# Kernel optimization log

Measured on AMD Instinct MI355X. Metric: run time of the kernel, lower is better.

The kernel has to match this reference:

```python
import jax, jax.numpy as jnp
import numpy as np

N = 100000
E = 3200000
F_IN = 16
H = 128
LAT = 64
L = 3
G = 1024


def setup_inputs() -> dict:
    key = jax.random.key(0)
    ks = jax.random.split(key, 12)
    x = jax.random.normal(ks[0], (N, F_IN), dtype=jnp.float32)
    edge_index = jax.random.randint(ks[1], (2, E), 0, N, dtype=jnp.int64)
    batch = jnp.sort(jax.random.randint(ks[2], (N,), 0, G, dtype=jnp.int64))
    batch = batch.at[-1].set(G - 1)  # ensure batch.max()+1 == G
    s_in = 1.0 / np.sqrt(F_IN)
    s_h = 1.0 / np.sqrt(H)
    W_in = jax.random.uniform(ks[3], (F_IN, H), jnp.float32, -s_in, s_in)
    b_in = jax.random.uniform(ks[4], (H,), jnp.float32, -s_in, s_in)
    W_msg = jax.random.uniform(ks[5], (L, H, H), jnp.float32, -s_h, s_h)
    b_msg = jax.random.uniform(ks[6], (L, H), jnp.float32, -s_h, s_h)
    W_mean = jax.random.uniform(ks[7], (H, LAT), jnp.float32, -s_h, s_h)
    b_mean = jax.random.uniform(ks[8], (LAT,), jnp.float32, -s_h, s_h)
    W_logvar = jax.random.uniform(ks[9], (H, LAT), jnp.float32, -s_h, s_h)
    b_logvar = jax.random.uniform(ks[10], (LAT,), jnp.float32, -s_h, s_h)
    return {
        "x": x, "edge_index": edge_index, "batch": batch, "num_graphs": G,
        "W_in": W_in, "b_in": b_in, "W_msg": W_msg, "b_msg": b_msg,
        "W_mean": W_mean, "b_mean": b_mean,
        "W_logvar": W_logvar, "b_logvar": b_logvar,
    }


def reference(x, edge_index, batch, num_graphs, W_in, b_in, W_msg, b_msg,
              W_mean, b_mean, W_logvar, b_logvar):
    src, dst = edge_index[0], edge_index[1]
    n = x.shape[0]
    # input net: Linear + ReLU
    h = jax.nn.relu(x @ W_in + b_in)  # [N, H]
    # stacked message-passing: transform, gather at src, scatter-add to dst, ReLU
    for l in range(L):
        m = h @ W_msg[l] + b_msg[l]                    # [N, H]
        agg = jax.ops.segment_sum(m[src], dst, num_segments=n)  # [N, H]
        h = jax.nn.relu(agg)
    # graph-level sum pooling via index_add over batch ids
    graph_embedding = jax.ops.segment_sum(h, batch, num_segments=num_graphs)  # [G, H]
    z_mean = graph_embedding @ W_mean + b_mean
    z_logvar = graph_embedding @ W_logvar + b_logvar
    return (z_mean, z_logvar)
```

## Files before the change

kernel.cpp:

```cpp
#include <hip/hip_runtime.h>

constexpr int N_  = 100000;
constexpr int E_  = 3200000;
constexpr int FIN = 16;
constexpr int H_  = 128;
constexpr int LAT = 64;
constexpr int L_  = 3;
constexpr int G_  = 1024;

constexpr int BSH = 9;
constexpr int BNODES = 1 << BSH;
constexpr int NB_ = (N_ + BNODES - 1) / BNODES;
constexpr int FILL_NB = 512;
constexpr int FILL_CHUNK = E_ / FILL_NB;

using bf16x8 = __attribute__((ext_vector_type(8))) short;
using f32x4  = __attribute__((ext_vector_type(4))) float;

__device__ inline float bflo(unsigned int u) {
  union { unsigned int i; float f; } v; v.i = u << 16; return v.f;
}
__device__ inline float bfhi(unsigned int u) {
  union { unsigned int i; float f; } v; v.i = u & 0xffff0000u; return v.f;
}
__device__ inline unsigned short f2bf(float f) {
  union { float f; unsigned int i; } v; v.f = f;
  unsigned int r = v.i + 0x7fffu + ((v.i >> 16) & 1u);
  return (unsigned short)(r >> 16);
}

__global__ __launch_bounds__(256) void k_wconv(const float* __restrict__ W,
                                               unsigned short* __restrict__ Wt,
                                               int* __restrict__ bcnt) {
  if (blockIdx.x == 0) {
    for (int i = threadIdx.x; i < NB_; i += 256) bcnt[i] = 0;
  }
  const int idx = blockIdx.x * 256 + threadIdx.x;
  if (idx < L_ * H_ * H_) {
    const int l = idx >> 14, rem = idx & 16383;
    const int c = rem >> 7, k = rem & 127;
    Wt[idx] = f2bf(W[l * H_ * H_ + k * H_ + c]);
  }
}

__global__ __launch_bounds__(256) void k_input(const float* __restrict__ x,
                                               const float* __restrict__ Win,
                                               const float* __restrict__ bin,
                                               unsigned short* __restrict__ h) {
  __shared__ float Wl[FIN * H_];
  __shared__ float xl[4 * FIN];
  const int tid = threadIdx.x;
  for (int i = tid; i < FIN * H_; i += 256) Wl[i] = Win[i];
  const int n0 = blockIdx.x * 4;
  if (tid < 4 * FIN) xl[tid] = x[(size_t)n0 * FIN + tid];
  __syncthreads();
  const int nl = tid >> 6, l = tid & 63;
  float a0 = bin[2 * l], a1 = bin[2 * l + 1];
#pragma unroll
  for (int k = 0; k < FIN; ++k) {
    const float xv = xl[nl * FIN + k];
    a0 += xv * Wl[k * H_ + 2 * l];
    a1 += xv * Wl[k * H_ + 2 * l + 1];
  }
  const unsigned int packed =
      (unsigned int)f2bf(fmaxf(a0, 0.f)) | ((unsigned int)f2bf(fmaxf(a1, 0.f)) << 16);
  *reinterpret_cast<unsigned int*>(h + (size_t)(n0 + nl) * H_ + 2 * l) = packed;
}

__global__ __launch_bounds__(256) void k_msg_mfma(const unsigned short* __restrict__ h,
                                                  const unsigned short* __restrict__ Wt,
                                                  const float* __restrict__ b,
                                                  unsigned short* __restrict__ m) {
  __shared__ unsigned short st[4][32][40];
  const int wave = threadIdx.x >> 6;
  const int lane = threadIdx.x & 63;
  const int r = lane & 15;
  const int g = lane >> 4;
  const int n0 = blockIdx.x * 32;
  const int cb = wave * 32;

  f32x4 acc[2][2] = {};
#pragma unroll
  for (int kk = 0; kk < 4; ++kk) {
    const int koff = kk * 32 + g * 8;
    const bf16x8 a0 = *reinterpret_cast<const bf16x8*>(h + (size_t)(n0 + r) * H_ + koff);
    const bf16x8 a1 = *reinterpret_cast<const bf16x8*>(h + (size_t)(n0 + 16 + r) * H_ + koff);
    const bf16x8 b0 = *reinterpret_cast<const bf16x8*>(Wt + (size_t)(cb + r) * H_ + koff);
    const bf16x8 b1 = *reinterpret_cast<const bf16x8*>(Wt + (size_t)(cb + 16 + r) * H_ + koff);
    acc[0][0] = __builtin_amdgcn_mfma_f32_16x16x32_bf16(a0, b0, acc[0][0], 0, 0, 0);
    acc[0][1] = __builtin_amdgcn_mfma_f32_16x16x32_bf16(a0, b1, acc[0][1], 0, 0, 0);
    acc[1][0] = __builtin_amdgcn_mfma_f32_16x16x32_bf16(a1, b0, acc[1][0], 0, 0, 0);
    acc[1][1] = __builtin_amdgcn_mfma_f32_16x16x32_bf16(a1, b1, acc[1][1], 0, 0, 0);
  }

  const float bc0 = b[cb + r];
  const float bc1 = b[cb + 16 + r];
#pragma unroll
  for (int rt = 0; rt < 2; ++rt)
#pragma unroll
    for (int ct = 0; ct < 2; ++ct) {
      const float bc = ct ? bc1 : bc0;
#pragma unroll
      for (int j = 0; j < 4; ++j)
        st[wave][rt * 16 + g * 4 + j][ct * 16 + r] = f2bf(acc[rt][ct][j] + bc);
    }
  __syncthreads();
#pragma unroll
  for (int p = 0; p < 2; ++p) {
    const int lr = p * 16 + (lane >> 2);
    const int seg = lane & 3;
    const bf16x8 v = *reinterpret_cast<const bf16x8*>(&st[wave][lr][seg * 8]);
    *reinterpret_cast<bf16x8*>(m + (size_t)(n0 + lr) * H_ + cb + seg * 8) = v;
  }
}

__global__ __launch_bounds__(256) void k_bhist(const int* __restrict__ ei,
                                               int* __restrict__ bcnt) {
  __shared__ int lh[NB_];
  for (int i = threadIdx.x; i < NB_; i += 256) lh[i] = 0;
  __syncthreads();
  const int gid = blockIdx.x * 256 + threadIdx.x;
  const int stride = gridDim.x * 256;
  for (int e = gid; e < E_; e += stride) atomicAdd(&lh[ei[E_ + e] >> BSH], 1);
  __syncthreads();
  for (int i = threadIdx.x; i < NB_; i += 256)
    if (lh[i]) atomicAdd(&bcnt[i], lh[i]);
}

__global__ __launch_bounds__(256) void k_bscan(const int* __restrict__ bcnt,
                                               int* __restrict__ boff,
                                               int* __restrict__ bcur,
                                               float* __restrict__ ge) {
  __shared__ int s[256];
  const int t = threadIdx.x;
  s[t] = (t < NB_) ? bcnt[t] : 0;
  __syncthreads();
  for (int off = 1; off < 256; off <<= 1) {
    const int add = (t >= off) ? s[t - off] : 0;
    __syncthreads();
    s[t] += add;
    __syncthreads();
  }
  const int ex = (t == 0) ? 0 : s[t - 1];
  if (t < NB_) { boff[t] = ex; bcur[t] = ex; }
  if (t == 0) boff[NB_] = s[NB_ - 1];
  float4 z = make_float4(0.f, 0.f, 0.f, 0.f);
  float4* g4 = reinterpret_cast<float4*>(ge);
  for (int i = t; i < G_ * H_ / 4; i += 256) g4[i] = z;
}

__global__ __launch_bounds__(256) void k_bfill(const int* __restrict__ ei,
                                               int* __restrict__ bcur,
                                               unsigned int* __restrict__ ebuf) {
  __shared__ int lh[NB_], lbase[NB_];
  const int t = threadIdx.x;
  for (int i = t; i < NB_; i += 256) lh[i] = 0;
  __syncthreads();
  const int e0 = blockIdx.x * FILL_CHUNK;
  const int e1 = e0 + FILL_CHUNK;
  for (int e = e0 + t; e < e1; e += 256) atomicAdd(&lh[ei[E_ + e] >> BSH], 1);
  __syncthreads();
  for (int i = t; i < NB_; i += 256) {
    const int c = lh[i];
    lbase[i] = c ? atomicAdd(&bcur[i], c) : 0;
  }
  __syncthreads();
  for (int i = t; i < NB_; i += 256) lh[i] = 0;
  __syncthreads();
  for (int e = e0 + t; e < e1; e += 256) {
    const int src = ei[e], dst = ei[E_ + e];
    const int b = dst >> BSH;
    const int pos = lbase[b] + atomicAdd(&lh[b], 1);
    ebuf[pos] = ((unsigned)src << BSH) | (unsigned)(dst & (BNODES - 1));
  }
}

__global__ __launch_bounds__(256) void k_bcsr(const unsigned int* __restrict__ ebuf,
                                              const int* __restrict__ boff,
                                              int* __restrict__ rowp,
                                              int* __restrict__ ssrc) {
  __shared__ int sdeg[BNODES];
  __shared__ int scur[BNODES];
  __shared__ int part[256];
  const int b = blockIdx.x;
  const int nbase = b << BSH;
  const int ncnt = min(BNODES, N_ - nbase);
  const int ebeg = boff[b], eend = boff[b + 1];
  const int t = threadIdx.x;
  for (int i = t; i < BNODES; i += 256) { sdeg[i] = 0; scur[i] = 0; }
  __syncthreads();
  for (int e = ebeg + t; e < eend; e += 256)
    atomicAdd(&sdeg[ebuf[e] & (BNODES - 1)], 1);
  __syncthreads();
  const int i0 = 2 * t, i1 = 2 * t + 1;
  const int d0 = sdeg[i0];
  part[t] = d0 + sdeg[i1];
  __syncthreads();
  for (int off = 1; off < 256; off <<= 1) {
    const int add = (t >= off) ? part[t - off] : 0;
    __syncthreads();
    part[t] += add;
    __syncthreads();
  }
  const int ex = (t == 0) ? 0 : part[t - 1];
  sdeg[i0] = ex;
  sdeg[i1] = ex + d0;
  __syncthreads();
  for (int i = t; i < ncnt; i += 256) rowp[nbase + i] = ebeg + sdeg[i];
  if (b == NB_ - 1 && t == 0) rowp[N_] = E_;
  for (int e = ebeg + t; e < eend; e += 256) {
    const unsigned int ed = ebuf[e];
    const int ld = ed & (BNODES - 1);
    const int pos = ebeg + sdeg[ld] + atomicAdd(&scur[ld], 1);
    ssrc[pos] = (int)(ed >> BSH);
  }
}

__global__ __launch_bounds__(256) void k_gather(const unsigned short* __restrict__ m,
                                                const int* __restrict__ rowptr,
                                                const int* __restrict__ ssrc,
                                                unsigned short* __restrict__ h) {
  const int n = blockIdx.x * 4 + (threadIdx.x >> 6);
  const int c2 = threadIdx.x & 63;
  const int beg = rowptr[n], end = rowptr[n + 1];
  const unsigned short* mc = m + 2 * c2;
  float a0 = 0.f, a1 = 0.f;
  int i = beg;
  for (; i + 15 < end; i += 16) {
    int s[16];
#pragma unroll
    for (int u = 0; u < 16; ++u) s[u] = ssrc[i + u];
    unsigned int v[16];
#pragma unroll
    for (int u = 0; u < 16; ++u)
      v[u] = *reinterpret_cast<const unsigned int*>(mc + (size_t)s[u] * H_);
#pragma unroll
    for (int u = 0; u < 16; ++u) { a0 += bflo(v[u]); a1 += bfhi(v[u]); }
  }
  for (; i + 3 < end; i += 4) {
    int s[4];
#pragma unroll
    for (int u = 0; u < 4; ++u) s[u] = ssrc[i + u];
    unsigned int v[4];
#pragma unroll
    for (int u = 0; u < 4; ++u)
      v[u] = *reinterpret_cast<const unsigned int*>(mc + (size_t)s[u] * H_);
#pragma unroll
    for (int u = 0; u < 4; ++u) { a0 += bflo(v[u]); a1 += bfhi(v[u]); }
  }
  for (; i < end; ++i) {
    const unsigned int v = *reinterpret_cast<const unsigned int*>(mc + (size_t)ssrc[i] * H_);
    a0 += bflo(v);  a1 += bfhi(v);
  }
  const unsigned int packed =
      (unsigned int)f2bf(fmaxf(a0, 0.f)) | ((unsigned int)f2bf(fmaxf(a1, 0.f)) << 16);
  *reinterpret_cast<unsigned int*>(h + (size_t)n * H_ + 2 * c2) = packed;
}

constexpr int POOL_CHUNK = 128;
__global__ __launch_bounds__(128) void k_pool(const unsigned short* __restrict__ h,
                                              const int* __restrict__ batch,
                                              float* __restrict__ ge) {
  __shared__ int bl[POOL_CHUNK];
  const int tid = threadIdx.x;
  const int start = blockIdx.x * POOL_CHUNK;
  const int cnt = min(POOL_CHUNK, N_ - start);
  if (tid < cnt) bl[tid] = batch[start + tid];
  __syncthreads();
  float run = 0.f;
  int cur = bl[0];
  for (int i = 0; i < cnt; ++i) {
    const int bid = bl[i];
    const float v = bflo((unsigned int)h[(size_t)(start + i) * H_ + tid]);
    if (bid != cur) {
      unsafeAtomicAdd(&ge[(size_t)cur * H_ + tid], run);
      run = 0.f;
      cur = bid;
    }
    run += v;
  }
  unsafeAtomicAdd(&ge[(size_t)cur * H_ + tid], run);
}

__global__ __launch_bounds__(128) void k_out(const float* __restrict__ ge,
                                             const float* __restrict__ Wm,
                                             const float* __restrict__ bm,
                                             const float* __restrict__ Wv,
                                             const float* __restrict__ bv,
                                             float* __restrict__ out) {
  __shared__ float gl[H_];
  const int g = blockIdx.x, tid = threadIdx.x;
  gl[tid] = ge[(size_t)g * H_ + tid];
  __syncthreads();
  const bool is_mean = (tid < LAT);
  const float* W = is_mean ? Wm : Wv;
  const float* bb = is_mean ? bm : bv;
  const int c = tid & 63;
  float acc = bb[c];
#pragma unroll 8
  for (int k = 0; k < H_; ++k) acc += gl[k] * W[k * LAT + c];
  const size_t off = is_mean ? 0 : (size_t)G_ * LAT;
  out[off + (size_t)g * LAT + c] = acc;
}

extern "C" void kernel_launch(void* const* d_in, const int* in_sizes, int n_in,
                              void* d_out, int out_size, void* d_ws, size_t ws_size,
                              hipStream_t stream) {
  const float* x     = (const float*)d_in[0];
  const int*   ei    = (const int*)d_in[1];
  const int*   batch = (const int*)d_in[2];
  const float* Win   = (const float*)d_in[4];
  const float* bin   = (const float*)d_in[5];
  const float* Wmsg  = (const float*)d_in[6];
  const float* bmsg  = (const float*)d_in[7];
  const float* Wmean = (const float*)d_in[8];
  const float* bmean = (const float*)d_in[9];
  const float* Wlv   = (const float*)d_in[10];
  const float* blv   = (const float*)d_in[11];
  float* out = (float*)d_out;

  char* p = (char*)d_ws;
  unsigned short* h  = (unsigned short*)p;  p += (size_t)N_ * H_ * 2;
  unsigned short* m  = (unsigned short*)p;  p += (size_t)N_ * H_ * 2;
  unsigned int* ebuf = (unsigned int*)p;    p += (size_t)E_ * 4;
  int* ssrc          = (int*)p;             p += (size_t)E_ * 4;
  int* rowp          = (int*)p;             p += (size_t)(N_ + 1) * 4;
  unsigned short* Wt = (unsigned short*)p;  p += (size_t)L_ * H_ * H_ * 2;
  float* ge          = (float*)p;           p += (size_t)G_ * H_ * 4;
  int* bcnt          = (int*)p;             p += (size_t)NB_ * 4;
  int* boff          = (int*)p;             p += (size_t)(NB_ + 1) * 4;
  int* bcur          = (int*)p;             p += (size_t)NB_ * 4;

  k_wconv<<<(L_ * H_ * H_ + 255) / 256, 256, 0, stream>>>(Wmsg, Wt, bcnt);

  k_bhist<<<256, 256, 0, stream>>>(ei, bcnt);
  k_bscan<<<1, 256, 0, stream>>>(bcnt, boff, bcur, ge);
  k_bfill<<<FILL_NB, 256, 0, stream>>>(ei, bcur, ebuf);
  k_bcsr<<<NB_, 256, 0, stream>>>(ebuf, boff, rowp, ssrc);

  k_input<<<N_ / 4, 256, 0, stream>>>(x, Win, bin, h);

  for (int l = 0; l < L_; ++l) {
    k_msg_mfma<<<N_ / 32, 256, 0, stream>>>(h, Wt + (size_t)l * H_ * H_,
                                            bmsg + (size_t)l * H_, m);
    k_gather<<<N_ / 4, 256, 0, stream>>>(m, rowp, ssrc, h);
  }

  k_pool<<<(N_ + POOL_CHUNK - 1) / POOL_CHUNK, 128, 0, stream>>>(h, batch, ge);

  k_out<<<G_, 128, 0, stream>>>(ge, Wmean, bmean, Wlv, blv, out);
}
```

Baseline: 559.3 us.

## Merge independent setup kernels and overlap CSR build with first message GEMM

Combines the edge-histogram, weight conversion and input projection into one heterogeneous k_init launch partitioned by block index. It also runs the per-bucket CSR build and the layer-0 message MFMA as disjoint block ranges of a single k_csrmsg launch, since they do not depend on each other. The bcnt zeroing moves to a hipMemsetAsync. The aim is fewer kernel launches and fewer idle tails between small dependent-free stages. In exchange the merged kernels carry larger shared-memory footprints and more branching, which may lower occupancy for the heavier parts.

```diff
diff --git a/kernel.cpp b/kernel.cpp
--- a/kernel.cpp
+++ b/kernel.cpp
@@ -14,6 +14,12 @@
 constexpr int FILL_NB = 512;
 constexpr int FILL_CHUNK = E_ / FILL_NB;
 
+constexpr int WCONV_BLOCKS = (L_ * H_ * H_) / 256;
+constexpr int BHIST_BLOCKS = 512;
+constexpr int INIT_WCONV0 = BHIST_BLOCKS;
+constexpr int INIT_INPUT0 = BHIST_BLOCKS + WCONV_BLOCKS;
+constexpr int MSG_BLOCKS = N_ / 32;
+
 using bf16x8 = __attribute__((ext_vector_type(8))) short;
 using f32x4  = __attribute__((ext_vector_type(4))) float;
 
@@ -29,29 +35,38 @@
   return (unsigned short)(r >> 16);
 }
 
-__global__ __launch_bounds__(256) void k_wconv(const float* __restrict__ W,
-                                               unsigned short* __restrict__ Wt,
-                                               int* __restrict__ bcnt) {
-  if (blockIdx.x == 0) {
-    for (int i = threadIdx.x; i < NB_; i += 256) bcnt[i] = 0;
-  }
-  const int idx = blockIdx.x * 256 + threadIdx.x;
-  if (idx < L_ * H_ * H_) {
+__global__ __launch_bounds__(256) void k_init(const int* __restrict__ ei,
+                                              int* __restrict__ bcnt,
+                                              const float* __restrict__ W,
+                                              unsigned short* __restrict__ Wt,
+                                              const float* __restrict__ x,
+                                              const float* __restrict__ Win,
+                                              const float* __restrict__ bin,
+                                              unsigned short* __restrict__ h) {
+  const int tid = threadIdx.x;
+  __shared__ int lh[NB_];
+  __shared__ float Wl[FIN * H_];
+  __shared__ float xl[4 * FIN];
+  if (blockIdx.x < BHIST_BLOCKS) {
+    for (int i = tid; i < NB_; i += 256) lh[i] = 0;
+    __syncthreads();
+    const int gid = blockIdx.x * 256 + tid;
+    const int stride = BHIST_BLOCKS * 256;
+    for (int e = gid; e < E_; e += stride) atomicAdd(&lh[ei[E_ + e] >> BSH], 1);
+    __syncthreads();
+    for (int i = tid; i < NB_; i += 256)
+      if (lh[i]) atomicAdd(&bcnt[i], lh[i]);
+    return;
+  }
+  if (blockIdx.x < INIT_INPUT0) {
+    const int idx = (blockIdx.x - INIT_WCONV0) * 256 + tid;
     const int l = idx >> 14, rem = idx & 16383;
     const int c = rem >> 7, k = rem & 127;
     Wt[idx] = f2bf(W[l * H_ * H_ + k * H_ + c]);
-  }
-}
-
-__global__ __launch_bounds__(256) void k_input(const float* __restrict__ x,
-                                               const float* __restrict__ Win,
-                                               const float* __restrict__ bin,
-                                               unsigned short* __restrict__ h) {
-  __shared__ float Wl[FIN * H_];
-  __shared__ float xl[4 * FIN];
-  const int tid = threadIdx.x;
+    return;
+  }
   for (int i = tid; i < FIN * H_; i += 256) Wl[i] = Win[i];
-  const int n0 = blockIdx.x * 4;
+  const int n0 = (blockIdx.x - INIT_INPUT0) * 4;
   if (tid < 4 * FIN) xl[tid] = x[(size_t)n0 * FIN + tid];
   __syncthreads();
   const int nl = tid >> 6, l = tid & 63;
@@ -67,16 +82,17 @@
   *reinterpret_cast<unsigned int*>(h + (size_t)(n0 + nl) * H_ + 2 * l) = packed;
 }
 
-__global__ __launch_bounds__(256) void k_msg_mfma(const unsigned short* __restrict__ h,
-                                                  const unsigned short* __restrict__ Wt,
-                                                  const float* __restrict__ b,
-                                                  unsigned short* __restrict__ m) {
-  __shared__ unsigned short st[4][32][40];
-  const int wave = threadIdx.x >> 6;
-  const int lane = threadIdx.x & 63;
+__device__ __forceinline__ void msg_body(int bid, int tid,
+                                         const unsigned short* __restrict__ h,
+                                         const unsigned short* __restrict__ Wt,
+                                         const float* __restrict__ b,
+                                         unsigned short* __restrict__ m,
+                                         unsigned short (*st)[32][40]) {
+  const int wave = tid >> 6;
+  const int lane = tid & 63;
   const int r = lane & 15;
   const int g = lane >> 4;
-  const int n0 = blockIdx.x * 32;
+  const int n0 = bid * 32;
   const int cb = wave * 32;
 
   f32x4 acc[2][2] = {};
@@ -114,17 +130,12 @@
   }
 }
 
-__global__ __launch_bounds__(256) void k_bhist(const int* __restrict__ ei,
-                                               int* __restrict__ bcnt) {
-  __shared__ int lh[NB_];
-  for (int i = threadIdx.x; i < NB_; i += 256) lh[i] = 0;
-  __syncthreads();
-  const int gid = blockIdx.x * 256 + threadIdx.x;
-  const int stride = gridDim.x * 256;
-  for (int e = gid; e < E_; e += stride) atomicAdd(&lh[ei[E_ + e] >> BSH], 1);
-  __syncthreads();
-  for (int i = threadIdx.x; i < NB_; i += 256)
-    if (lh[i]) atomicAdd(&bcnt[i], lh[i]);
+__global__ __launch_bounds__(256) void k_msg_mfma(const unsigned short* __restrict__ h,
+                                                  const unsigned short* __restrict__ Wt,
+                                                  const float* __restrict__ b,
+                                                  unsigned short* __restrict__ m) {
+  __shared__ unsigned short st[4][32][40];
+  msg_body(blockIdx.x, threadIdx.x, h, Wt, b, m, st);
 }
 
 __global__ __launch_bounds__(256) void k_bscan(const int* __restrict__ bcnt,
@@ -175,18 +186,27 @@
   }
 }
 
-__global__ __launch_bounds__(256) void k_bcsr(const unsigned int* __restrict__ ebuf,
-                                              const int* __restrict__ boff,
-                                              int* __restrict__ rowp,
-                                              int* __restrict__ ssrc) {
+__global__ __launch_bounds__(256) void k_csrmsg(const unsigned int* __restrict__ ebuf,
+                                                const int* __restrict__ boff,
+                                                int* __restrict__ rowp,
+                                                int* __restrict__ ssrc,
+                                                const unsigned short* __restrict__ h,
+                                                const unsigned short* __restrict__ Wt,
+                                                const float* __restrict__ bb,
+                                                unsigned short* __restrict__ m) {
   __shared__ int sdeg[BNODES];
   __shared__ int scur[BNODES];
   __shared__ int part[256];
+  __shared__ unsigned short st[4][32][40];
+  const int t = threadIdx.x;
+  if (blockIdx.x >= NB_) {
+    msg_body(blockIdx.x - NB_, t, h, Wt, bb, m, st);
+    return;
+  }
   const int b = blockIdx.x;
   const int nbase = b << BSH;
   const int ncnt = min(BNODES, N_ - nbase);
   const int ebeg = boff[b], eend = boff[b + 1];
-  const int t = threadIdx.x;
   for (int i = t; i < BNODES; i += 256) { sdeg[i] = 0; scur[i] = 0; }
   __syncthreads();
   for (int e = ebeg + t; e < eend; e += 256)
@@ -331,22 +351,22 @@
   int* boff          = (int*)p;             p += (size_t)(NB_ + 1) * 4;
   int* bcur          = (int*)p;             p += (size_t)NB_ * 4;
 
-  k_wconv<<<(L_ * H_ * H_ + 255) / 256, 256, 0, stream>>>(Wmsg, Wt, bcnt);
-
-  k_bhist<<<256, 256, 0, stream>>>(ei, bcnt);
+  hipMemsetAsync(bcnt, 0, (size_t)NB_ * sizeof(int), stream);
+  k_init<<<INIT_INPUT0 + N_ / 4, 256, 0, stream>>>(ei, bcnt, Wmsg, Wt, x, Win, bin, h);
+
   k_bscan<<<1, 256, 0, stream>>>(bcnt, boff, bcur, ge);
   k_bfill<<<FILL_NB, 256, 0, stream>>>(ei, bcur, ebuf);
-  k_bcsr<<<NB_, 256, 0, stream>>>(ebuf, boff, rowp, ssrc);
-
-  k_input<<<N_ / 4, 256, 0, stream>>>(x, Win, bin, h);
-
-  for (int l = 0; l < L_; ++l) {
-    k_msg_mfma<<<N_ / 32, 256, 0, stream>>>(h, Wt + (size_t)l * H_ * H_,
-                                            bmsg + (size_t)l * H_, m);
-    k_gather<<<N_ / 4, 256, 0, stream>>>(m, rowp, ssrc, h);
-  }
+  k_csrmsg<<<NB_ + MSG_BLOCKS, 256, 0, stream>>>(ebuf, boff, rowp, ssrc,
+                                                 h, Wt, bmsg, m);
+
+  k_gather<<<N_ / 4, 256, 0, stream>>>(m, rowp, ssrc, h);
+  k_msg_mfma<<<MSG_BLOCKS, 256, 0, stream>>>(h, Wt + (size_t)H_ * H_,
+                                             bmsg + H_, m);
+  k_gather<<<N_ / 4, 256, 0, stream>>>(m, rowp, ssrc, h);
+  k_msg_mfma<<<MSG_BLOCKS, 256, 0, stream>>>(h, Wt + (size_t)2 * H_ * H_,
+                                             bmsg + 2 * H_, m);
+  k_gather<<<N_ / 4, 256, 0, stream>>>(m, rowp, ssrc, h);
 
   k_pool<<<(N_ + POOL_CHUNK - 1) / POOL_CHUNK, 128, 0, stream>>>(h, batch, ge);
-
   k_out<<<G_, 128, 0, stream>>>(ge, Wmean, bmean, Wlv, blv, out);
 }
```

After: 544.3 us. 1.03x faster.
